# Performance work log

Hardware: AMD Instinct MI355X
Metric: run time of the kernel (lower is better)

The kernel has to match this reference:

```python
import jax, jax.numpy as jnp
import numpy as np
from jax import lax

S = 48          # fixed crop size (original crops are ragged; fixed here for batching)
EPS = 0.1       # Sinkhorn entropic regularization
ITERS = 50      # Sinkhorn iterations
TINY = 1e-8


def setup_inputs() -> dict:
    key = jax.random.key(0)
    k1, k2, k3 = jax.random.split(key, 3)
    B, C, H, W = 16, 5, 160, 160
    hm_gt = jax.random.uniform(k1, (B, C, H, W), dtype=jnp.float32)
    hm_pred = jax.random.uniform(k2, (B, C, H, W), dtype=jnp.float32)
    tops = jax.random.randint(k3, (B, 8, 2), 0, 112, dtype=jnp.int32)  # (y, x) per rect
    return {"hm_gt": hm_gt, "hm_pred": hm_pred, "tops": tops}


def _geometry_distance(s):
    # pairwise Euclidean distance between pixel centers of an s x s crop -> [s*s, s*s]
    ys, xs = jnp.meshgrid(jnp.arange(s, dtype=jnp.float32),
                          jnp.arange(s, dtype=jnp.float32), indexing="ij")
    pts = jnp.stack([ys.ravel(), xs.ravel()], axis=-1)          # [s*s, 2]
    d2 = jnp.sum((pts[:, None, :] - pts[None, :, :]) ** 2, -1)  # [s*s, s*s]
    return jnp.sqrt(d2)


def _crop_all(hm, tops):
    # hm: [B, C, H, W], tops: [B, R, 2] -> crops [B, R, C, S, S]
    def crop_one(hm_b, top):  # hm_b [C,H,W], top [2]
        return lax.dynamic_slice(hm_b, (0, top[0], top[1]), (hm_b.shape[0], S, S))
    return jax.vmap(lambda hb, tb: jax.vmap(lambda t: crop_one(hb, t))(tb))(hm, tops)


def reference(hm_gt, hm_pred, tops):
    B, C, H, W = hm_gt.shape
    n = S * S
    dist = _geometry_distance(S)            # [n, n]
    K = jnp.exp(-dist / EPS)                # Gibbs kernel
    M = K * dist                            # for the transport cost readout

    a = _crop_all(hm_gt, tops).reshape(-1, n)    # [N, n]
    b = _crop_all(hm_pred, tops).reshape(-1, n)  # [N, n]
    a = a / (jnp.sum(a, -1, keepdims=True) + TINY)   # normalize to marginals
    b = b / (jnp.sum(b, -1, keepdims=True) + TINY)

    N = a.shape[0]
    u0 = jnp.full((N, n), 1.0 / n, dtype=a.dtype)
    v0 = jnp.full((N, n), 1.0 / n, dtype=a.dtype)

    def body(carry, _):
        u, v = carry
        v = b / (u @ K + TINY)      # [N,n] @ [n,n]
        u = a / (v @ K.T + TINY)
        return (u, v), None

    (u, v), _ = lax.scan(body, (u0, v0), None, length=ITERS)
    # loss per crop: sum_ij u_i K_ij dist_ij v_j
    loss = jnp.sum((u @ M) * v)
    return loss
```

## Files before the change

kernel.cpp:

```cpp
#include <hip/hip_runtime.h>

#define TINYF 1e-8f
#define NITER 50

typedef __attribute__((ext_vector_type(2))) float v2f;

__device__ __forceinline__ float wWs(float v) {
    return __int_as_float(__builtin_amdgcn_update_dpp(0, __float_as_int(v), 0x138, 0xf, 0xf, true));
}
__device__ __forceinline__ float wEs(float v) {
    return __int_as_float(__builtin_amdgcn_update_dpp(0, __float_as_int(v), 0x130, 0xf, 0xf, true));
}
__device__ __forceinline__ v2f wW(v2f v) { v2f r; r.x = wWs(v.x); r.y = wWs(v.y); return r; }
__device__ __forceinline__ v2f wE(v2f v) { v2f r; r.x = wEs(v.x); r.y = wEs(v.y); return r; }
__device__ __forceinline__ v2f rcp2(v2f v) {
    v2f r; r.x = __builtin_amdgcn_rcpf(v.x); r.y = __builtin_amdgcn_rcpf(v.y); return r;
}
__device__ __forceinline__ v2f pfma(float k, v2f a, v2f c) {
    v2f kv; kv.x = k; kv.y = k;
    return __builtin_elementwise_fma(kv, a, c);
}

__global__ void __launch_bounds__(256)
sinkhorn_plq(const float* __restrict__ hm_gt,
             const float* __restrict__ hm_pred,
             const int* __restrict__ tops,
             float* __restrict__ out) {
    __shared__ v2f ES[2][6][4][64];
    __shared__ float sred[2][4];

    const int t = threadIdx.x;
    const int W = t >> 6;
    const int l = t & 63;
    const bool act = (l < 48);

    {
        const int p = W >> 1, r = W & 1;
        ((float*)&ES[p][0][2 + r][l])[0] = 0.f;
        ((float*)&ES[p][5][r][l])[1] = 0.f;
    }

    const int blk = blockIdx.x;
    const int bi = blk / 40, rr = (blk / 5) % 8, cc = blk % 5;
    const int y0 = tops[(bi * 8 + rr) * 2 + 0];
    const int x0 = tops[(bi * 8 + rr) * 2 + 1];
    const float* srcA = hm_gt + (size_t)(bi * 5 + cc) * 25600;
    const float* srcB = hm_pred + (size_t)(bi * 5 + cc) * 25600;

    v2f va[6], vb[6];
    float sA = 0.f, sB = 0.f;
    const int rbx = y0 + 6 * W;
    const int rby = y0 + 24 + 6 * W;
#pragma unroll
    for (int r = 0; r < 6; ++r) {
        const int gx = (rbx + r) * 160 + x0 + l;
        const int gy = (rby + r) * 160 + x0 + l;
        va[r].x = act ? srcA[gx] : 0.f;
        va[r].y = act ? srcA[gy] : 0.f;
        vb[r].x = act ? srcB[gx] : 0.f;
        vb[r].y = act ? srcB[gy] : 0.f;
        sA += va[r].x + va[r].y;
        sB += vb[r].x + vb[r].y;
    }
#pragma unroll
    for (int o = 1; o < 64; o <<= 1) {
        sA += __shfl_xor(sA, o, 64);
        sB += __shfl_xor(sB, o, 64);
    }
    if (l == 0) { sred[0][W] = sA; sred[1][W] = sB; }
    __syncthreads();
    sA = sred[0][0] + sred[0][1] + sred[0][2] + sred[0][3];
    sB = sred[1][0] + sred[1][1] + sred[1][2] + sred[1][3];
    const float nA = 1.0f / (sA + TINYF);
    const float nB = 1.0f / (sB + TINYF);
#pragma unroll
    for (int r = 0; r < 6; ++r) {
        va[r].x *= nA; va[r].y *= nA;
        vb[r].x *= nB; vb[r].y *= nB;
    }

    const float e10 = expf(-1.0f / 0.1f);
    const float e2  = expf(-sqrtf(2.0f) / 0.1f);
    const float e20 = expf(-2.0f / 0.1f);
    const v2f tiny = {TINYF, TINYF};

    v2f xu[6], xv[6];
    const float u0 = 1.0f / 2304.0f;
#pragma unroll
    for (int r = 0; r < 6; ++r) { xu[r].x = act ? u0 : 0.f; xu[r].y = act ? u0 : 0.f; }

    v2f s1o[6], s2o[6];
    auto prep = [&](const v2f (&x)[6]) {
#pragma unroll
        for (int r = 0; r < 6; ++r) {
            const v2f w1 = wW(x[r]), e1 = wE(x[r]);
            s1o[r] = w1 + e1;
            s2o[r] = wW(w1) + wE(e1);
        }
    };

    auto half = [&](const v2f (&x)[6], v2f (&o)[6], const v2f (&co)[6],
                    int p, int q) {
        const v2f um1 = ES[p][W][3][l];
        const v2f up6 = ES[p][W + 2][0][l];
        const v2f um2 = ES[p][W][2][l];
        const v2f up7 = ES[p][W + 2][1][l];
        v2f a;
        a = x[2];
        a = pfma(e10, s1o[2] + (x[1] + x[3]), a);
        a = pfma(e2,  s1o[1] + s1o[3], a);
        a = pfma(e20, s2o[2] + (x[0] + x[4]), a);
        o[2] = co[2] * rcp2(a + tiny);
        a = x[3];
        a = pfma(e10, s1o[3] + (x[2] + x[4]), a);
        a = pfma(e2,  s1o[2] + s1o[4], a);
        a = pfma(e20, s2o[3] + (x[1] + x[5]), a);
        o[3] = co[3] * rcp2(a + tiny);
        a = x[1];
        a = pfma(e10, s1o[1] + (x[0] + x[2]), a);
        a = pfma(e2,  s1o[0] + s1o[2], a);
        a = pfma(e20, s2o[1] + (um1 + x[3]), a);
        o[1] = co[1] * rcp2(a + tiny);
        ES[q][W + 1][1][l] = o[1];
        a = x[4];
        a = pfma(e10, s1o[4] + (x[3] + x[5]), a);
        a = pfma(e2,  s1o[3] + s1o[5], a);
        a = pfma(e20, s2o[4] + (x[2] + up6), a);
        o[4] = co[4] * rcp2(a + tiny);
        ES[q][W + 1][2][l] = o[4];
        const v2f s1m = wW(um1) + wE(um1);
        const v2f s1p = wW(up6) + wE(up6);
        a = x[0];
        a = pfma(e10, s1o[0] + (um1 + x[1]), a);
        a = pfma(e2,  s1m + s1o[1], a);
        a = pfma(e20, s2o[0] + (um2 + x[2]), a);
        o[0] = co[0] * rcp2(a + tiny);
        ES[q][W + 1][0][l] = o[0];
        a = x[5];
        a = pfma(e10, s1o[5] + (x[4] + up6), a);
        a = pfma(e2,  s1o[4] + s1p, a);
        a = pfma(e20, s2o[5] + (x[3] + up7), a);
        o[5] = co[5] * rcp2(a + tiny);
        ES[q][W + 1][3][l] = o[5];
        if (W == 3) {
            ((float*)&ES[q][0][2][l])[1] = o[4].x;
            ((float*)&ES[q][0][3][l])[1] = o[5].x;
        }
        if (W == 0) {
            ((float*)&ES[q][5][0][l])[0] = o[0].y;
            ((float*)&ES[q][5][1][l])[0] = o[1].y;
        }
        prep(o);
    };

    {
        ES[0][W + 1][0][l] = xu[0];
        ES[0][W + 1][1][l] = xu[1];
        ES[0][W + 1][2][l] = xu[4];
        ES[0][W + 1][3][l] = xu[5];
        if (W == 3) {
            ((float*)&ES[0][0][2][l])[1] = xu[4].x;
            ((float*)&ES[0][0][3][l])[1] = xu[5].x;
        }
        if (W == 0) {
            ((float*)&ES[0][5][0][l])[0] = xu[0].y;
            ((float*)&ES[0][5][1][l])[0] = xu[1].y;
        }
        prep(xu);
        __syncthreads();
    }

#pragma unroll 1
    for (int it = 0; it < NITER; ++it) {
        half(xu, xv, vb, 0, 1);
        __syncthreads();
        half(xv, xu, va, 1, 0);
        __syncthreads();
    }

    const float s2f = sqrtf(2.0f);
    const float m01 = e10, m02 = e20 * 2.0f, m11 = e2 * s2f;
    v2f ls = {0.f, 0.f};
    {
        const v2f um1 = ES[0][W][3][l];
        const v2f up6 = ES[0][W + 2][0][l];
        const v2f um2 = ES[0][W][2][l];
        const v2f up7 = ES[0][W + 2][1][l];
        const v2f s1m = wW(um1) + wE(um1);
        const v2f s1p = wW(up6) + wE(up6);
        const v2f zero = {0.f, 0.f};
        v2f a;
        a = pfma(m01, s1o[0] + (um1 + xu[1]), zero);
        a = pfma(m11, s1m + s1o[1], a);
        a = pfma(m02, s2o[0] + (um2 + xu[2]), a);
        ls += a * xv[0];
        a = pfma(m01, s1o[1] + (xu[0] + xu[2]), zero);
        a = pfma(m11, s1o[0] + s1o[2], a);
        a = pfma(m02, s2o[1] + (um1 + xu[3]), a);
        ls += a * xv[1];
        a = pfma(m01, s1o[2] + (xu[1] + xu[3]), zero);
        a = pfma(m11, s1o[1] + s1o[3], a);
        a = pfma(m02, s2o[2] + (xu[0] + xu[4]), a);
        ls += a * xv[2];
        a = pfma(m01, s1o[3] + (xu[2] + xu[4]), zero);
        a = pfma(m11, s1o[2] + s1o[4], a);
        a = pfma(m02, s2o[3] + (xu[1] + xu[5]), a);
        ls += a * xv[3];
        a = pfma(m01, s1o[4] + (xu[3] + xu[5]), zero);
        a = pfma(m11, s1o[3] + s1o[5], a);
        a = pfma(m02, s2o[4] + (xu[2] + up6), a);
        ls += a * xv[4];
        a = pfma(m01, s1o[5] + (xu[4] + up6), zero);
        a = pfma(m11, s1o[4] + s1p, a);
        a = pfma(m02, s2o[5] + (xu[3] + up7), a);
        ls += a * xv[5];
    }
    float lsum = ls.x + ls.y;

#pragma unroll
    for (int o = 1; o < 64; o <<= 1) lsum += __shfl_xor(lsum, o, 64);
    if (l == 0) sred[0][W] = lsum;
    __syncthreads();
    if (t == 0)
        atomicAdd(out, sred[0][0] + sred[0][1] + sred[0][2] + sred[0][3]);
}

extern "C" void kernel_launch(void* const* d_in, const int* in_sizes, int n_in,
                              void* d_out, int out_size, void* d_ws, size_t ws_size,
                              hipStream_t stream) {
    (void)in_sizes; (void)n_in; (void)out_size; (void)d_ws; (void)ws_size;
    const float* hm_gt = (const float*)d_in[0];
    const float* hm_pred = (const float*)d_in[1];
    const int* tops = (const int*)d_in[2];
    float* out = (float*)d_out;

    hipMemsetAsync(out, 0, sizeof(float), stream);
    sinkhorn_plq<<<dim3(640), dim3(256), 0, stream>>>(hm_gt, hm_pred, tops, out);
}
```

Before: 166.9 us.

## Split each crop across eight waves with three row-pairs each

```diff
diff --git a/kernel.cpp b/kernel.cpp
--- a/kernel.cpp
+++ b/kernel.cpp
@@ -21,23 +21,25 @@
     return __builtin_elementwise_fma(kv, a, c);
 }
 
-__global__ void __launch_bounds__(256)
-sinkhorn_plq(const float* __restrict__ hm_gt,
+__global__ void __launch_bounds__(512)
+sinkhorn_8w3(const float* __restrict__ hm_gt,
              const float* __restrict__ hm_pred,
              const int* __restrict__ tops,
              float* __restrict__ out) {
-    __shared__ v2f ES[2][6][4][64];
-    __shared__ float sred[2][4];
+    __shared__ v2f ES[2][10][4][64];
+    __shared__ float sred[2][8];
 
     const int t = threadIdx.x;
     const int W = t >> 6;
     const int l = t & 63;
     const bool act = (l < 48);
 
-    {
+    if (W < 4) {
         const int p = W >> 1, r = W & 1;
         ((float*)&ES[p][0][2 + r][l])[0] = 0.f;
-        ((float*)&ES[p][5][r][l])[1] = 0.f;
+    } else {
+        const int p = (W - 4) >> 1, r = W & 1;
+        ((float*)&ES[p][9][r][l])[1] = 0.f;
     }
 
     const int blk = blockIdx.x;
@@ -47,12 +49,12 @@
     const float* srcA = hm_gt + (size_t)(bi * 5 + cc) * 25600;
     const float* srcB = hm_pred + (size_t)(bi * 5 + cc) * 25600;
 
-    v2f va[6], vb[6];
+    v2f va[3], vb[3];
     float sA = 0.f, sB = 0.f;
-    const int rbx = y0 + 6 * W;
-    const int rby = y0 + 24 + 6 * W;
-#pragma unroll
-    for (int r = 0; r < 6; ++r) {
+    const int rbx = y0 + 3 * W;
+    const int rby = y0 + 24 + 3 * W;
+#pragma unroll
+    for (int r = 0; r < 3; ++r) {
         const int gx = (rbx + r) * 160 + x0 + l;
         const int gy = (rby + r) * 160 + x0 + l;
         va[r].x = act ? srcA[gx] : 0.f;
@@ -69,12 +71,13 @@
     }
     if (l == 0) { sred[0][W] = sA; sred[1][W] = sB; }
     __syncthreads();
-    sA = sred[0][0] + sred[0][1] + sred[0][2] + sred[0][3];
-    sB = sred[1][0] + sred[1][1] + sred[1][2] + sred[1][3];
+    sA = 0.f; sB = 0.f;
+#pragma unroll
+    for (int w = 0; w < 8; ++w) { sA += sred[0][w]; sB += sred[1][w]; }
     const float nA = 1.0f / (sA + TINYF);
     const float nB = 1.0f / (sB + TINYF);
 #pragma unroll
-    for (int r = 0; r < 6; ++r) {
+    for (int r = 0; r < 3; ++r) {
         va[r].x *= nA; va[r].y *= nA;
         vb[r].x *= nB; vb[r].y *= nB;
     }
@@ -84,91 +87,78 @@
     const float e20 = expf(-2.0f / 0.1f);
     const v2f tiny = {TINYF, TINYF};
 
-    v2f xu[6], xv[6];
+    v2f xu[3], xv[3];
     const float u0 = 1.0f / 2304.0f;
 #pragma unroll
-    for (int r = 0; r < 6; ++r) { xu[r].x = act ? u0 : 0.f; xu[r].y = act ? u0 : 0.f; }
-
-    v2f s1o[6], s2o[6];
-    auto prep = [&](const v2f (&x)[6]) {
-#pragma unroll
-        for (int r = 0; r < 6; ++r) {
+    for (int r = 0; r < 3; ++r) { xu[r].x = act ? u0 : 0.f; xu[r].y = act ? u0 : 0.f; }
+
+    v2f s1o[3], s2o[3];
+    auto prep = [&](const v2f (&x)[3]) {
+#pragma unroll
+        for (int r = 0; r < 3; ++r) {
             const v2f w1 = wW(x[r]), e1 = wE(x[r]);
             s1o[r] = w1 + e1;
             s2o[r] = wW(w1) + wE(e1);
         }
     };
 
-    auto half = [&](const v2f (&x)[6], v2f (&o)[6], const v2f (&co)[6],
+    auto publish = [&](const v2f (&y)[3], int q) {
+        ES[q][W + 1][0][l] = y[0];
+        ES[q][W + 1][1][l] = y[1];
+        ES[q][W + 1][2][l] = y[1];
+        ES[q][W + 1][3][l] = y[2];
+        if (W == 7) {
+            ((float*)&ES[q][0][2][l])[1] = y[1].x;
+            ((float*)&ES[q][0][3][l])[1] = y[2].x;
+        }
+        if (W == 0) {
+            ((float*)&ES[q][9][0][l])[0] = y[0].y;
+            ((float*)&ES[q][9][1][l])[0] = y[1].y;
+        }
+    };
+
+    auto half = [&](const v2f (&x)[3], v2f (&o)[3], const v2f (&co)[3],
                     int p, int q) {
+        const v2f um2 = ES[p][W][2][l];
         const v2f um1 = ES[p][W][3][l];
-        const v2f up6 = ES[p][W + 2][0][l];
-        const v2f um2 = ES[p][W][2][l];
-        const v2f up7 = ES[p][W + 2][1][l];
+        const v2f hp3 = ES[p][W + 2][0][l];
+        const v2f hp4 = ES[p][W + 2][1][l];
         v2f a;
-        a = x[2];
-        a = pfma(e10, s1o[2] + (x[1] + x[3]), a);
-        a = pfma(e2,  s1o[1] + s1o[3], a);
-        a = pfma(e20, s2o[2] + (x[0] + x[4]), a);
-        o[2] = co[2] * rcp2(a + tiny);
-        a = x[3];
-        a = pfma(e10, s1o[3] + (x[2] + x[4]), a);
-        a = pfma(e2,  s1o[2] + s1o[4], a);
-        a = pfma(e20, s2o[3] + (x[1] + x[5]), a);
-        o[3] = co[3] * rcp2(a + tiny);
         a = x[1];
         a = pfma(e10, s1o[1] + (x[0] + x[2]), a);
         a = pfma(e2,  s1o[0] + s1o[2], a);
-        a = pfma(e20, s2o[1] + (um1 + x[3]), a);
+        a = pfma(e20, s2o[1] + (um1 + hp3), a);
         o[1] = co[1] * rcp2(a + tiny);
         ES[q][W + 1][1][l] = o[1];
-        a = x[4];
-        a = pfma(e10, s1o[4] + (x[3] + x[5]), a);
-        a = pfma(e2,  s1o[3] + s1o[5], a);
-        a = pfma(e20, s2o[4] + (x[2] + up6), a);
-        o[4] = co[4] * rcp2(a + tiny);
-        ES[q][W + 1][2][l] = o[4];
+        ES[q][W + 1][2][l] = o[1];
         const v2f s1m = wW(um1) + wE(um1);
-        const v2f s1p = wW(up6) + wE(up6);
+        const v2f s1p = wW(hp3) + wE(hp3);
         a = x[0];
         a = pfma(e10, s1o[0] + (um1 + x[1]), a);
         a = pfma(e2,  s1m + s1o[1], a);
         a = pfma(e20, s2o[0] + (um2 + x[2]), a);
         o[0] = co[0] * rcp2(a + tiny);
         ES[q][W + 1][0][l] = o[0];
-        a = x[5];
-        a = pfma(e10, s1o[5] + (x[4] + up6), a);
-        a = pfma(e2,  s1o[4] + s1p, a);
-        a = pfma(e20, s2o[5] + (x[3] + up7), a);
-        o[5] = co[5] * rcp2(a + tiny);
-        ES[q][W + 1][3][l] = o[5];
-        if (W == 3) {
-            ((float*)&ES[q][0][2][l])[1] = o[4].x;
-            ((float*)&ES[q][0][3][l])[1] = o[5].x;
+        a = x[2];
+        a = pfma(e10, s1o[2] + (x[1] + hp3), a);
+        a = pfma(e2,  s1o[1] + s1p, a);
+        a = pfma(e20, s2o[2] + (x[0] + hp4), a);
+        o[2] = co[2] * rcp2(a + tiny);
+        ES[q][W + 1][3][l] = o[2];
+        if (W == 7) {
+            ((float*)&ES[q][0][2][l])[1] = o[1].x;
+            ((float*)&ES[q][0][3][l])[1] = o[2].x;
         }
         if (W == 0) {
-            ((float*)&ES[q][5][0][l])[0] = o[0].y;
-            ((float*)&ES[q][5][1][l])[0] = o[1].y;
+            ((float*)&ES[q][9][0][l])[0] = o[0].y;
+            ((float*)&ES[q][9][1][l])[0] = o[1].y;
         }
         prep(o);
     };
 
-    {
-        ES[0][W + 1][0][l] = xu[0];
-        ES[0][W + 1][1][l] = xu[1];
-        ES[0][W + 1][2][l] = xu[4];
-        ES[0][W + 1][3][l] = xu[5];
-        if (W == 3) {
-            ((float*)&ES[0][0][2][l])[1] = xu[4].x;
-            ((float*)&ES[0][0][3][l])[1] = xu[5].x;
-        }
-        if (W == 0) {
-            ((float*)&ES[0][5][0][l])[0] = xu[0].y;
-            ((float*)&ES[0][5][1][l])[0] = xu[1].y;
-        }
-        prep(xu);
-        __syncthreads();
-    }
+    publish(xu, 0);
+    prep(xu);
+    __syncthreads();
 
 #pragma unroll 1
     for (int it = 0; it < NITER; ++it) {
@@ -182,12 +172,12 @@
     const float m01 = e10, m02 = e20 * 2.0f, m11 = e2 * s2f;
     v2f ls = {0.f, 0.f};
     {
+        const v2f um2 = ES[0][W][2][l];
         const v2f um1 = ES[0][W][3][l];
-        const v2f up6 = ES[0][W + 2][0][l];
-        const v2f um2 = ES[0][W][2][l];
-        const v2f up7 = ES[0][W + 2][1][l];
+        const v2f hp3 = ES[0][W + 2][0][l];
+        const v2f hp4 = ES[0][W + 2][1][l];
         const v2f s1m = wW(um1) + wE(um1);
-        const v2f s1p = wW(up6) + wE(up6);
+        const v2f s1p = wW(hp3) + wE(hp3);
         const v2f zero = {0.f, 0.f};
         v2f a;
         a = pfma(m01, s1o[0] + (um1 + xu[1]), zero);
@@ -196,24 +186,12 @@
         ls += a * xv[0];
         a = pfma(m01, s1o[1] + (xu[0] + xu[2]), zero);
         a = pfma(m11, s1o[0] + s1o[2], a);
-        a = pfma(m02, s2o[1] + (um1 + xu[3]), a);
+        a = pfma(m02, s2o[1] + (um1 + hp3), a);
         ls += a * xv[1];
-        a = pfma(m01, s1o[2] + (xu[1] + xu[3]), zero);
-        a = pfma(m11, s1o[1] + s1o[3], a);
-        a = pfma(m02, s2o[2] + (xu[0] + xu[4]), a);
+        a = pfma(m01, s1o[2] + (xu[1] + hp3), zero);
+        a = pfma(m11, s1o[1] + s1p, a);
+        a = pfma(m02, s2o[2] + (xu[0] + hp4), a);
         ls += a * xv[2];
-        a = pfma(m01, s1o[3] + (xu[2] + xu[4]), zero);
-        a = pfma(m11, s1o[2] + s1o[4], a);
-        a = pfma(m02, s2o[3] + (xu[1] + xu[5]), a);
-        ls += a * xv[3];
-        a = pfma(m01, s1o[4] + (xu[3] + xu[5]), zero);
-        a = pfma(m11, s1o[3] + s1o[5], a);
-        a = pfma(m02, s2o[4] + (xu[2] + up6), a);
-        ls += a * xv[4];
-        a = pfma(m01, s1o[5] + (xu[4] + up6), zero);
-        a = pfma(m11, s1o[4] + s1p, a);
-        a = pfma(m02, s2o[5] + (xu[3] + up7), a);
-        ls += a * xv[5];
     }
     float lsum = ls.x + ls.y;
 
@@ -221,8 +199,12 @@
     for (int o = 1; o < 64; o <<= 1) lsum += __shfl_xor(lsum, o, 64);
     if (l == 0) sred[0][W] = lsum;
     __syncthreads();
-    if (t == 0)
-        atomicAdd(out, sred[0][0] + sred[0][1] + sred[0][2] + sred[0][3]);
+    if (t == 0) {
+        float s = 0.f;
+#pragma unroll
+        for (int w = 0; w < 8; ++w) s += sred[0][w];
+        atomicAdd(out, s);
+    }
 }
 
 extern "C" void kernel_launch(void* const* d_in, const int* in_sizes, int n_in,
@@ -235,5 +217,5 @@
     float* out = (float*)d_out;
 
     hipMemsetAsync(out, 0, sizeof(float), stream);
-    sinkhorn_plq<<<dim3(640), dim3(256), 0, stream>>>(hm_gt, hm_pred, tops, out);
-}
+    sinkhorn_8w3<<<dim3(640), dim3(512), 0, stream>>>(hm_gt, hm_pred, tops, out);
+}
```

Result: slower. 172.8 us (+3.5%).
